# Kernel tuning notes

Measured on AMD Instinct MI355X. Metric: run time of the kernel, lower is better.

Reference implementation:

```python
import jax, jax.numpy as jnp
import numpy as np

B, T, D_IN, P, Q, D_OUT = 128, 1024, 64, 128, 2, 64


def _lstm_layer(x, w_ih, w_hh, b):
    """One LSTM layer, batch_first. x: [B,T,Din], w_ih: [4P,Din], w_hh: [4P,P], b: [4P].
    PyTorch gate order: i, f, g, o."""
    # Precompute input contribution for all timesteps (the big, parallel GEMM).
    gx = jnp.einsum('btd,gd->btg', x, w_ih) + b          # [B,T,4P]
    gx_t = jnp.swapaxes(gx, 0, 1)                        # [T,B,4P] for scan
    p = w_hh.shape[1]
    h0 = jnp.zeros((x.shape[0], p), dtype=x.dtype)
    c0 = jnp.zeros((x.shape[0], p), dtype=x.dtype)

    def step(carry, g_in):
        h, c = carry
        g = g_in + h @ w_hh.T                            # [B,4P]
        i, f, gg, o = jnp.split(g, 4, axis=-1)
        i = jax.nn.sigmoid(i)
        f = jax.nn.sigmoid(f)
        gg = jnp.tanh(gg)
        o = jax.nn.sigmoid(o)
        c = f * c + i * gg
        h = o * jnp.tanh(c)
        return (h, c), h

    _, hs = jax.lax.scan(step, (h0, c0), gx_t)           # hs: [T,B,P]
    return jnp.swapaxes(hs, 0, 1)                        # [B,T,P]


def setup_inputs() -> dict:
    key = jax.random.key(0)
    ks = jax.random.split(key, 8)
    x = jax.random.normal(ks[0], (B, T, D_IN), dtype=jnp.float32)
    # weight_ih: kaiming-normal-ish; weight_hh: orthogonal-ish (random normal is a fine stand-in
    # numerically; init distribution doesn't change the math being tested).
    w_ih0 = jax.random.normal(ks[1], (4 * P, D_IN), dtype=jnp.float32) * (1.0 / np.sqrt(D_IN))
    w_hh0 = jax.random.normal(ks[2], (4 * P, P), dtype=jnp.float32) * (1.0 / np.sqrt(P))
    w_ih1 = jax.random.normal(ks[3], (4 * P, P), dtype=jnp.float32) * (1.0 / np.sqrt(P))
    w_hh1 = jax.random.normal(ks[4], (4 * P, P), dtype=jnp.float32) * (1.0 / np.sqrt(P))
    # biases initialized to zero in the original (bias_ih + bias_hh folded into one per layer
    # would be equivalent math; keep both for faithfulness)
    b_ih = jnp.zeros((Q, 4 * P), dtype=jnp.float32)
    b_hh = jnp.zeros((Q, 4 * P), dtype=jnp.float32)
    fc_w = jax.random.normal(ks[5], (D_OUT, P), dtype=jnp.float32) * np.sqrt(2.0 / P)
    fc_b = jnp.zeros((D_OUT,), dtype=jnp.float32)
    return {"x": x, "w_ih0": w_ih0, "w_hh0": w_hh0, "w_ih1": w_ih1, "w_hh1": w_hh1,
            "b_ih": b_ih, "b_hh": b_hh, "fc_w": fc_w, "fc_b": fc_b}


def reference(x, w_ih0, w_hh0, w_ih1, w_hh1, b_ih, b_hh, fc_w, fc_b):
    h = _lstm_layer(x, w_ih0, w_hh0, b_ih[0] + b_hh[0])   # layer 0: [B,T,P]
    h = _lstm_layer(h, w_ih1, w_hh1, b_ih[1] + b_hh[1])   # layer 1: [B,T,P]
    return jnp.einsum('btp,op->bto', h, fc_w) + fc_b      # [B,T,D_OUT]
```

## Files before the change

kernel.cpp:

```cpp
#include <hip/hip_runtime.h>

#define NT 1024
#define RINGS 256

typedef _Float16 half8 __attribute__((ext_vector_type(8)));
typedef _Float16 half4 __attribute__((ext_vector_type(4)));
typedef float f32x4 __attribute__((ext_vector_type(4)));
typedef unsigned long long u64;
struct U2 { u64 a, b; };

#ifndef __has_builtin
#define __has_builtin(x) 0
#endif

__device__ __forceinline__ f32x4 MFMA(half8 a, half8 b, f32x4 c) {
  return __builtin_amdgcn_mfma_f32_16x16x32_f16(a, b, c, 0, 0, 0);
}
__device__ __forceinline__ float exp2h(float x) {
#if __has_builtin(__builtin_amdgcn_exp2f)
  return __builtin_amdgcn_exp2f(x);
#else
  return exp2f(x);
#endif
}
__device__ __forceinline__ float sigf(float x) {
  return __builtin_amdgcn_rcpf(1.0f + exp2h(x * -1.44269504f));
}
__device__ __forceinline__ float tanhf2(float x) {
  float t = __builtin_amdgcn_rcpf(1.0f + exp2h(x * 2.88539008f));
  return fmaf(-2.0f, t, 1.0f);
}
__device__ __forceinline__ half8 cvt8(float4 c0, float4 c1) {
  half8 hv;
  hv[0] = (_Float16)c0.x; hv[1] = (_Float16)c0.y;
  hv[2] = (_Float16)c0.z; hv[3] = (_Float16)c0.w;
  hv[4] = (_Float16)c1.x; hv[5] = (_Float16)c1.y;
  hv[6] = (_Float16)c1.z; hv[7] = (_Float16)c1.w;
  return hv;
}
__device__ __forceinline__ half8 ldring(const _Float16* p) {
  const u64* q = (const u64*)p;
  U2 uu;
  uu.a = __hip_atomic_load(q, __ATOMIC_RELAXED, __HIP_MEMORY_SCOPE_AGENT);
  uu.b = __hip_atomic_load(q + 1, __ATOMIC_RELAXED, __HIP_MEMORY_SCOPE_AGENT);
  return __builtin_bit_cast(half8, uu);
}
__device__ __forceinline__ unsigned wpoll(unsigned* p, unsigned tgt,
                                          unsigned cached, int l) {
  unsigned c = cached;
  while (c < tgt) {
    unsigned pv = 0;
    if (l == 0)
      pv = __hip_atomic_load(p, __ATOMIC_ACQUIRE, __HIP_MEMORY_SCOPE_AGENT);
    c = (unsigned)__builtin_amdgcn_readfirstlane((int)pv);
    if (c < tgt) __builtin_amdgcn_s_sleep(2);
  }
  return c;
}

__global__ __launch_bounds__(256) void prep_x(const float* __restrict__ x,
                                              _Float16* __restrict__ Xf) {
  int t0 = blockIdx.x * 256 + threadIdx.x;
  int l = t0 & 63;
  int fid = t0 >> 6;
  int kt = fid & 1;
  int t = (fid >> 1) & (NT - 1);
  int g = fid >> 11;
  int bt = g * 16 + (l & 15);
  int kb = kt * 32 + (l >> 4) * 4;
  const float* src = x + ((size_t)bt * NT + (size_t)t) * 64 + kb;
  float4 v0 = *(const float4*)src;
  float4 v1 = *(const float4*)(src + 16);
  *(half8*)(Xf + (size_t)fid * 512 + l * 8) = cvt8(v0, v1);
}

__global__ __launch_bounds__(512, 1) void lstm_main(
    const float* __restrict__ wih0, const float* __restrict__ whh0,
    const float* __restrict__ wih1, const float* __restrict__ whh1,
    const float* __restrict__ bih, const float* __restrict__ bhh,
    const float* __restrict__ fcw, const float* __restrict__ fcb,
    const _Float16* __restrict__ Xf, _Float16* __restrict__ ringH0,
    unsigned* __restrict__ flags, float* __restrict__ out) {
  const int tid = threadIdx.x;
  const int w = tid >> 6, l = tid & 63;
  const int n = l & 15, lg = l >> 4;
  const bool producer = blockIdx.x < 8;
  const int g = blockIdx.x & 7;

  __shared__ _Float16 hfr[2][4][64][8];
  __shared__ _Float16 fcl[4][4][64][8];

  _Float16* ringG = ringH0 + (size_t)g * RINGS * 2048;
  unsigned* prog = flags + g * 16;
  unsigned* cons = flags + (8 + g) * 16;
  const half8 hz = {0, 0, 0, 0, 0, 0, 0, 0};

  if (producer) {
    half8 A[4][6];
    f32x4 bias[4];
#pragma unroll
    for (int q = 0; q < 4; ++q) {
      int row = (w + 8 * q) * 16 + n;
#pragma unroll
      for (int kt = 0; kt < 2; ++kt) {
        const float* wp = wih0 + (size_t)row * 64 + kt * 32 + lg * 4;
        A[q][kt] = cvt8(*(const float4*)wp, *(const float4*)(wp + 16));
      }
#pragma unroll
      for (int kt = 0; kt < 4; ++kt) {
        const float* wp = whh0 + (size_t)row * 128 + kt * 32 + lg * 4;
        A[q][2 + kt] = cvt8(*(const float4*)wp, *(const float4*)(wp + 16));
      }
      int rb = (w + 8 * q) * 16 + lg * 4;
      f32x4 bv;
#pragma unroll
      for (int r = 0; r < 4; ++r) bv[r] = bih[rb + r] + bhh[rb + r];
      bias[q] = bv;
    }
    if (tid < 256) ((half8*)&hfr[1][0][0][0])[tid] = hz;
    const _Float16* XfG = Xf + (size_t)g * NT * 1024;
    f32x4 cst = {0.f, 0.f, 0.f, 0.f};
    unsigned Cc = 0;
    half8 x0 = *(const half8*)(XfG + l * 8);
    half8 x1 = *(const half8*)(XfG + 512 + l * 8);
    f32x4 xs0 = MFMA(A[0][0], x0, bias[0]);
    f32x4 xs1 = MFMA(A[1][0], x0, bias[1]);
    f32x4 xs2 = MFMA(A[2][0], x0, bias[2]);
    f32x4 xs3 = MFMA(A[3][0], x0, bias[3]);
    xs0 = MFMA(A[0][1], x1, xs0); xs1 = MFMA(A[1][1], x1, xs1);
    xs2 = MFMA(A[2][1], x1, xs2); xs3 = MFMA(A[3][1], x1, xs3);
    half8 xC0 = *(const half8*)(XfG + 1024 + l * 8);
    half8 xC1 = *(const half8*)(XfG + 1024 + 512 + l * 8);
    __syncthreads();
    for (int s = 0; s < NT; ++s) {
      if (s >= 224 && (s & 31) == 0)
        Cc = wpoll(cons, (unsigned)(s - 192), Cc, l);
      const int rdk = (s + 1) & 1;
      half8 b2 = *(const half8*)&hfr[rdk][0][l][0];
      half8 b3 = *(const half8*)&hfr[rdk][1][l][0];
      half8 b4 = *(const half8*)&hfr[rdk][2][l][0];
      half8 b5 = *(const half8*)&hfr[rdk][3][l][0];
      f32x4 hc0 = MFMA(A[0][2], b2, xs0);
      f32x4 hc1 = MFMA(A[1][2], b2, xs1);
      f32x4 hc2 = MFMA(A[2][2], b2, xs2);
      f32x4 hc3 = MFMA(A[3][2], b2, xs3);
      hc0 = MFMA(A[0][3], b3, hc0); hc1 = MFMA(A[1][3], b3, hc1);
      hc2 = MFMA(A[2][3], b3, hc2); hc3 = MFMA(A[3][3], b3, hc3);
      hc0 = MFMA(A[0][4], b4, hc0); hc1 = MFMA(A[1][4], b4, hc1);
      hc2 = MFMA(A[2][4], b4, hc2); hc3 = MFMA(A[3][4], b4, hc3);
      hc0 = MFMA(A[0][5], b5, hc0); hc1 = MFMA(A[1][5], b5, hc1);
      hc2 = MFMA(A[2][5], b5, hc2); hc3 = MFMA(A[3][5], b5, hc3);
      if (s + 1 < NT) {
        xs0 = MFMA(A[0][0], xC0, bias[0]);
        xs1 = MFMA(A[1][0], xC0, bias[1]);
        xs2 = MFMA(A[2][0], xC0, bias[2]);
        xs3 = MFMA(A[3][0], xC0, bias[3]);
        xs0 = MFMA(A[0][1], xC1, xs0); xs1 = MFMA(A[1][1], xC1, xs1);
        xs2 = MFMA(A[2][1], xC1, xs2); xs3 = MFMA(A[3][1], xC1, xs3);
      }
      if (s + 2 < NT) {
        const _Float16* p = XfG + (size_t)(s + 2) * 1024 + l * 8;
        xC0 = *(const half8*)p;
        xC1 = *(const half8*)(p + 512);
      }
      half4 hh;
#pragma unroll
      for (int r = 0; r < 4; ++r) {
        float iv = sigf(hc0[r]), fv = sigf(hc1[r]);
        float gv = tanhf2(hc2[r]), ov = sigf(hc3[r]);
        cst[r] = fv * cst[r] + iv * gv;
        hh[r] = (_Float16)(ov * tanhf2(cst[r]));
      }
      *(half4*)&hfr[s & 1][w >> 1][l][(w & 1) << 2] = hh;
      {
        u64 uh = __builtin_bit_cast(u64, hh);
        __hip_atomic_store(
            (u64*)(ringG + (size_t)(s & (RINGS - 1)) * 2048 +
                   (w >> 1) * 512 + l * 8 + (w & 1) * 4),
            uh, __ATOMIC_RELAXED, __HIP_MEMORY_SCOPE_AGENT);
      }
      asm volatile("s_waitcnt lgkmcnt(0)" ::: "memory");
      __builtin_amdgcn_sched_barrier(0);
      __builtin_amdgcn_s_barrier();
      __builtin_amdgcn_sched_barrier(0);
      if ((s & 31) == 31) {
        asm volatile("s_waitcnt vmcnt(0)" ::: "memory");
        __builtin_amdgcn_sched_barrier(0);
        __builtin_amdgcn_s_barrier();
        __builtin_amdgcn_sched_barrier(0);
        if (tid == 0)
          __hip_atomic_store(prog, (unsigned)(s + 1), __ATOMIC_RELEASE,
                             __HIP_MEMORY_SCOPE_AGENT);
      }
    }
  } else {
    half8 A[4][8];
    f32x4 bias[4], fcbv = {0.f, 0.f, 0.f, 0.f};
#pragma unroll
    for (int q = 0; q < 4; ++q) {
      int row = (w + 8 * q) * 16 + n;
#pragma unroll
      for (int kt = 0; kt < 4; ++kt) {
        const float* wp = wih1 + (size_t)row * 128 + kt * 32 + lg * 4;
        A[q][kt] = cvt8(*(const float4*)wp, *(const float4*)(wp + 16));
      }
#pragma unroll
      for (int kt = 0; kt < 4; ++kt) {
        const float* wp = whh1 + (size_t)row * 128 + kt * 32 + lg * 4;
        A[q][4 + kt] = cvt8(*(const float4*)wp, *(const float4*)(wp + 16));
      }
      int rb = (w + 8 * q) * 16 + lg * 4;
      f32x4 bv;
#pragma unroll
      for (int r = 0; r < 4; ++r)
        bv[r] = bih[512 + rb + r] + bhh[512 + rb + r];
      bias[q] = bv;
    }
    if (w < 4) {
      int frow = (w << 4) + n;
#pragma unroll
      for (int kt = 0; kt < 4; ++kt) {
        const float* wp = fcw + (size_t)frow * 128 + kt * 32 + lg * 4;
        *(half8*)&fcl[w][kt][l][0] =
            cvt8(*(const float4*)wp, *(const float4*)(wp + 16));
      }
      fcbv = *(const f32x4*)(fcb + (w << 4) + lg * 4);
    }
    if (tid < 256) ((half8*)&hfr[1][0][0][0])[tid] = hz;
    float* outG = out + (size_t)((g << 4) + n) * NT * 64 + (w << 4) + lg * 4;
    f32x4 cst = {0.f, 0.f, 0.f, 0.f};
    __syncthreads();
    unsigned Pc = wpoll(prog, 2u, 0u, l);
    half8 t0 = ldring(ringG + l * 8);
    half8 t1 = ldring(ringG + 512 + l * 8);
    half8 t2 = ldring(ringG + 1024 + l * 8);
    half8 t3 = ldring(ringG + 1536 + l * 8);
    f32x4 is0 = MFMA(A[0][0], t0, bias[0]);
    f32x4 is1 = MFMA(A[1][0], t0, bias[1]);
    f32x4 is2 = MFMA(A[2][0], t0, bias[2]);
    f32x4 is3 = MFMA(A[3][0], t0, bias[3]);
    is0 = MFMA(A[0][1], t1, is0); is1 = MFMA(A[1][1], t1, is1);
    is2 = MFMA(A[2][1], t1, is2); is3 = MFMA(A[3][1], t1, is3);
    is0 = MFMA(A[0][2], t2, is0); is1 = MFMA(A[1][2], t2, is1);
    is2 = MFMA(A[2][2], t2, is2); is3 = MFMA(A[3][2], t2, is3);
    is0 = MFMA(A[0][3], t3, is0); is1 = MFMA(A[1][3], t3, is1);
    is2 = MFMA(A[2][3], t3, is2); is3 = MFMA(A[3][3], t3, is3);
    const _Float16* rb1 = ringG + 2048 + l * 8;
    half8 HC0 = ldring(rb1);
    half8 HC1 = ldring(rb1 + 512);
    half8 HC2 = ldring(rb1 + 1024);
    half8 HC3 = ldring(rb1 + 1536);
    for (int t = 0; t < NT; ++t) {
      const int rdk = (t + 1) & 1;
      half8 b4 = *(const half8*)&hfr[rdk][0][l][0];
      half8 b5 = *(const half8*)&hfr[rdk][1][l][0];
      half8 b6 = *(const half8*)&hfr[rdk][2][l][0];
      half8 b7 = *(const half8*)&hfr[rdk][3][l][0];
      f32x4 hc0 = MFMA(A[0][4], b4, is0);
      f32x4 hc1 = MFMA(A[1][4], b4, is1);
      f32x4 hc2 = MFMA(A[2][4], b4, is2);
      f32x4 hc3 = MFMA(A[3][4], b4, is3);
      hc0 = MFMA(A[0][5], b5, hc0); hc1 = MFMA(A[1][5], b5, hc1);
      hc2 = MFMA(A[2][5], b5, hc2); hc3 = MFMA(A[3][5], b5, hc3);
      hc0 = MFMA(A[0][6], b6, hc0); hc1 = MFMA(A[1][6], b6, hc1);
      hc2 = MFMA(A[2][6], b6, hc2); hc3 = MFMA(A[3][6], b6, hc3);
      hc0 = MFMA(A[0][7], b7, hc0); hc1 = MFMA(A[1][7], b7, hc1);
      hc2 = MFMA(A[2][7], b7, hc2); hc3 = MFMA(A[3][7], b7, hc3);
      if (w < 4) {
        half8 f0 = *(const half8*)&fcl[w][0][l][0];
        half8 f1 = *(const half8*)&fcl[w][1][l][0];
        half8 f2 = *(const half8*)&fcl[w][2][l][0];
        half8 f3 = *(const half8*)&fcl[w][3][l][0];
        f32x4 afc = fcbv;
        afc = MFMA(f0, b4, afc); afc = MFMA(f1, b5, afc);
        afc = MFMA(f2, b6, afc); afc = MFMA(f3, b7, afc);
        if (t >= 1) *(f32x4*)(outG + (size_t)(t - 1) * 64) = afc;
      }
      if (t + 1 < NT) {
        is0 = MFMA(A[0][0], HC0, bias[0]);
        is1 = MFMA(A[1][0], HC0, bias[1]);
        is2 = MFMA(A[2][0], HC0, bias[2]);
        is3 = MFMA(A[3][0], HC0, bias[3]);
        is0 = MFMA(A[0][1], HC1, is0); is1 = MFMA(A[1][1], HC1, is1);
        is2 = MFMA(A[2][1], HC1, is2); is3 = MFMA(A[3][1], HC1, is3);
        is0 = MFMA(A[0][2], HC2, is0); is1 = MFMA(A[1][2], HC2, is1);
        is2 = MFMA(A[2][2], HC2, is2); is3 = MFMA(A[3][2], HC2, is3);
        is0 = MFMA(A[0][3], HC3, is0); is1 = MFMA(A[1][3], HC3, is1);
        is2 = MFMA(A[2][3], HC3, is2); is3 = MFMA(A[3][3], HC3, is3);
      }
      if (t + 2 < NT) {
        Pc = wpoll(prog, (unsigned)(t + 3), Pc, l);
        const _Float16* rb_ =
            ringG + (size_t)((t + 2) & (RINGS - 1)) * 2048 + l * 8;
        HC0 = ldring(rb_);
        HC1 = ldring(rb_ + 512);
        HC2 = ldring(rb_ + 1024);
        HC3 = ldring(rb_ + 1536);
      }
      half4 hh;
#pragma unroll
      for (int r = 0; r < 4; ++r) {
        float iv = sigf(hc0[r]), fv = sigf(hc1[r]);
        float gv = tanhf2(hc2[r]), ov = sigf(hc3[r]);
        cst[r] = fv * cst[r] + iv * gv;
        hh[r] = (_Float16)(ov * tanhf2(cst[r]));
      }
      *(half4*)&hfr[t & 1][w >> 1][l][(w & 1) << 2] = hh;
      if (tid == 0 && (t & 31) == 0)
        __hip_atomic_store(cons, (unsigned)t, __ATOMIC_RELAXED,
                           __HIP_MEMORY_SCOPE_AGENT);
      asm volatile("s_waitcnt lgkmcnt(0)" ::: "memory");
      __builtin_amdgcn_sched_barrier(0);
      __builtin_amdgcn_s_barrier();
      __builtin_amdgcn_sched_barrier(0);
    }
    {
      half8 b4 = *(const half8*)&hfr[(NT + 1) & 1][0][l][0];
      half8 b5 = *(const half8*)&hfr[(NT + 1) & 1][1][l][0];
      half8 b6 = *(const half8*)&hfr[(NT + 1) & 1][2][l][0];
      half8 b7 = *(const half8*)&hfr[(NT + 1) & 1][3][l][0];
      if (w < 4) {
        half8 f0 = *(const half8*)&fcl[w][0][l][0];
        half8 f1 = *(const half8*)&fcl[w][1][l][0];
        half8 f2 = *(const half8*)&fcl[w][2][l][0];
        half8 f3 = *(const half8*)&fcl[w][3][l][0];
        f32x4 afc = fcbv;
        afc = MFMA(f0, b4, afc); afc = MFMA(f1, b5, afc);
        afc = MFMA(f2, b6, afc); afc = MFMA(f3, b7, afc);
        *(f32x4*)(outG + (size_t)(NT - 1) * 64) = afc;
      }
    }
  }
}

extern "C" void kernel_launch(void* const* d_in, const int* in_sizes, int n_in,
                              void* d_out, int out_size, void* d_ws, size_t ws_size,
                              hipStream_t stream) {
  const float* x     = (const float*)d_in[0];
  const float* w_ih0 = (const float*)d_in[1];
  const float* w_hh0 = (const float*)d_in[2];
  const float* w_ih1 = (const float*)d_in[3];
  const float* w_hh1 = (const float*)d_in[4];
  const float* b_ih  = (const float*)d_in[5];
  const float* b_hh  = (const float*)d_in[6];
  const float* fc_w  = (const float*)d_in[7];
  const float* fc_b  = (const float*)d_in[8];

  _Float16* Xf   = (_Float16*)d_ws;
  _Float16* ring = (_Float16*)((char*)d_ws + (16u << 20));
  unsigned* flags = (unsigned*)((char*)d_ws + (24u << 20));

  hipMemsetAsync(flags, 0, 4096, stream);
  prep_x<<<4096, 256, 0, stream>>>(x, Xf);
  lstm_main<<<16, 512, 0, stream>>>(w_ih0, w_hh0, w_ih1, w_hh1, b_ih, b_hh,
                                    fc_w, fc_b, Xf, ring, flags,
                                    (float*)d_out);
}
```

Baseline: 1.328 ms.

## Split each block into input-projection and recurrent warp groups via LDS handoff

Result: slower. 1.616 ms (+21.7%).

```diff
diff --git a/kernel.cpp b/kernel.cpp
--- a/kernel.cpp
+++ b/kernel.cpp
@@ -74,7 +74,13 @@
   *(half8*)(Xf + (size_t)fid * 512 + l * 8) = cvt8(v0, v1);
 }
 
-__global__ __launch_bounds__(512, 1) void lstm_main(
+#define BARRIER_LGKM()                              \
+  asm volatile("s_waitcnt lgkmcnt(0)" ::: "memory"); \
+  __builtin_amdgcn_sched_barrier(0);                 \
+  __builtin_amdgcn_s_barrier();                      \
+  __builtin_amdgcn_sched_barrier(0)
+
+__global__ __launch_bounds__(1024, 1) void lstm_main(
     const float* __restrict__ wih0, const float* __restrict__ whh0,
     const float* __restrict__ wih1, const float* __restrict__ whh1,
     const float* __restrict__ bih, const float* __restrict__ bhh,
@@ -86,248 +92,294 @@
   const int n = l & 15, lg = l >> 4;
   const bool producer = blockIdx.x < 8;
   const int g = blockIdx.x & 7;
+  const int q = w & 7;
 
   __shared__ _Float16 hfr[2][4][64][8];
-  __shared__ _Float16 fcl[4][4][64][8];
+  __shared__ float pp[2][8][4][64][4];
 
   _Float16* ringG = ringH0 + (size_t)g * RINGS * 2048;
   unsigned* prog = flags + g * 16;
   unsigned* cons = flags + (8 + g) * 16;
   const half8 hz = {0, 0, 0, 0, 0, 0, 0, 0};
 
+  if (tid < 256) ((half8*)&hfr[1][0][0][0])[tid] = hz;
+
   if (producer) {
-    half8 A[4][6];
-    f32x4 bias[4];
-#pragma unroll
-    for (int q = 0; q < 4; ++q) {
-      int row = (w + 8 * q) * 16 + n;
-#pragma unroll
-      for (int kt = 0; kt < 2; ++kt) {
-        const float* wp = wih0 + (size_t)row * 64 + kt * 32 + lg * 4;
-        A[q][kt] = cvt8(*(const float4*)wp, *(const float4*)(wp + 16));
-      }
-#pragma unroll
-      for (int kt = 0; kt < 4; ++kt) {
-        const float* wp = whh0 + (size_t)row * 128 + kt * 32 + lg * 4;
-        A[q][2 + kt] = cvt8(*(const float4*)wp, *(const float4*)(wp + 16));
-      }
-      int rb = (w + 8 * q) * 16 + lg * 4;
-      f32x4 bv;
-#pragma unroll
-      for (int r = 0; r < 4; ++r) bv[r] = bih[rb + r] + bhh[rb + r];
-      bias[q] = bv;
-    }
-    if (tid < 256) ((half8*)&hfr[1][0][0][0])[tid] = hz;
-    const _Float16* XfG = Xf + (size_t)g * NT * 1024;
-    f32x4 cst = {0.f, 0.f, 0.f, 0.f};
-    unsigned Cc = 0;
-    half8 x0 = *(const half8*)(XfG + l * 8);
-    half8 x1 = *(const half8*)(XfG + 512 + l * 8);
-    f32x4 xs0 = MFMA(A[0][0], x0, bias[0]);
-    f32x4 xs1 = MFMA(A[1][0], x0, bias[1]);
-    f32x4 xs2 = MFMA(A[2][0], x0, bias[2]);
-    f32x4 xs3 = MFMA(A[3][0], x0, bias[3]);
-    xs0 = MFMA(A[0][1], x1, xs0); xs1 = MFMA(A[1][1], x1, xs1);
-    xs2 = MFMA(A[2][1], x1, xs2); xs3 = MFMA(A[3][1], x1, xs3);
-    half8 xC0 = *(const half8*)(XfG + 1024 + l * 8);
-    half8 xC1 = *(const half8*)(XfG + 1024 + 512 + l * 8);
-    __syncthreads();
-    for (int s = 0; s < NT; ++s) {
-      if (s >= 224 && (s & 31) == 0)
-        Cc = wpoll(cons, (unsigned)(s - 192), Cc, l);
-      const int rdk = (s + 1) & 1;
-      half8 b2 = *(const half8*)&hfr[rdk][0][l][0];
-      half8 b3 = *(const half8*)&hfr[rdk][1][l][0];
-      half8 b4 = *(const half8*)&hfr[rdk][2][l][0];
-      half8 b5 = *(const half8*)&hfr[rdk][3][l][0];
-      f32x4 hc0 = MFMA(A[0][2], b2, xs0);
-      f32x4 hc1 = MFMA(A[1][2], b2, xs1);
-      f32x4 hc2 = MFMA(A[2][2], b2, xs2);
-      f32x4 hc3 = MFMA(A[3][2], b2, xs3);
-      hc0 = MFMA(A[0][3], b3, hc0); hc1 = MFMA(A[1][3], b3, hc1);
-      hc2 = MFMA(A[2][3], b3, hc2); hc3 = MFMA(A[3][3], b3, hc3);
-      hc0 = MFMA(A[0][4], b4, hc0); hc1 = MFMA(A[1][4], b4, hc1);
-      hc2 = MFMA(A[2][4], b4, hc2); hc3 = MFMA(A[3][4], b4, hc3);
-      hc0 = MFMA(A[0][5], b5, hc0); hc1 = MFMA(A[1][5], b5, hc1);
-      hc2 = MFMA(A[2][5], b5, hc2); hc3 = MFMA(A[3][5], b5, hc3);
-      if (s + 1 < NT) {
-        xs0 = MFMA(A[0][0], xC0, bias[0]);
-        xs1 = MFMA(A[1][0], xC0, bias[1]);
-        xs2 = MFMA(A[2][0], xC0, bias[2]);
-        xs3 = MFMA(A[3][0], xC0, bias[3]);
-        xs0 = MFMA(A[0][1], xC1, xs0); xs1 = MFMA(A[1][1], xC1, xs1);
-        xs2 = MFMA(A[2][1], xC1, xs2); xs3 = MFMA(A[3][1], xC1, xs3);
-      }
-      if (s + 2 < NT) {
-        const _Float16* p = XfG + (size_t)(s + 2) * 1024 + l * 8;
-        xC0 = *(const half8*)p;
-        xC1 = *(const half8*)(p + 512);
-      }
-      half4 hh;
-#pragma unroll
-      for (int r = 0; r < 4; ++r) {
-        float iv = sigf(hc0[r]), fv = sigf(hc1[r]);
-        float gv = tanhf2(hc2[r]), ov = sigf(hc3[r]);
-        cst[r] = fv * cst[r] + iv * gv;
-        hh[r] = (_Float16)(ov * tanhf2(cst[r]));
-      }
-      *(half4*)&hfr[s & 1][w >> 1][l][(w & 1) << 2] = hh;
+    if (w < 8) {
+      half8 Ax[4][2];
+      f32x4 bias[4];
+#pragma unroll
+      for (int gt = 0; gt < 4; ++gt) {
+        int row = (q + 8 * gt) * 16 + n;
+#pragma unroll
+        for (int kt = 0; kt < 2; ++kt) {
+          const float* wp = wih0 + (size_t)row * 64 + kt * 32 + lg * 4;
+          Ax[gt][kt] = cvt8(*(const float4*)wp, *(const float4*)(wp + 16));
+        }
+        int rb = (q + 8 * gt) * 16 + lg * 4;
+        f32x4 bv;
+#pragma unroll
+        for (int r = 0; r < 4; ++r) bv[r] = bih[rb + r] + bhh[rb + r];
+        bias[gt] = bv;
+      }
+      const _Float16* XfG = Xf + (size_t)g * NT * 1024;
+      half8 xv0 = *(const half8*)(XfG + l * 8);
+      half8 xv1 = *(const half8*)(XfG + 512 + l * 8);
       {
+        f32x4 a0 = MFMA(Ax[0][0], xv0, bias[0]);
+        f32x4 a1 = MFMA(Ax[1][0], xv0, bias[1]);
+        f32x4 a2 = MFMA(Ax[2][0], xv0, bias[2]);
+        f32x4 a3 = MFMA(Ax[3][0], xv0, bias[3]);
+        a0 = MFMA(Ax[0][1], xv1, a0); a1 = MFMA(Ax[1][1], xv1, a1);
+        a2 = MFMA(Ax[2][1], xv1, a2); a3 = MFMA(Ax[3][1], xv1, a3);
+        *(f32x4*)&pp[0][q][0][l][0] = a0;
+        *(f32x4*)&pp[0][q][1][l][0] = a1;
+        *(f32x4*)&pp[0][q][2][l][0] = a2;
+        *(f32x4*)&pp[0][q][3][l][0] = a3;
+      }
+      xv0 = *(const half8*)(XfG + 1024 + l * 8);
+      xv1 = *(const half8*)(XfG + 1024 + 512 + l * 8);
+      unsigned Cc = 0;
+      __syncthreads();
+      for (int s = 0; s < NT; ++s) {
+        if (s >= 224 && (s & 31) == 0)
+          Cc = wpoll(cons, (unsigned)(s - 192), Cc, l);
+        if (s + 1 < NT) {
+          f32x4 a0 = MFMA(Ax[0][0], xv0, bias[0]);
+          f32x4 a1 = MFMA(Ax[1][0], xv0, bias[1]);
+          f32x4 a2 = MFMA(Ax[2][0], xv0, bias[2]);
+          f32x4 a3 = MFMA(Ax[3][0], xv0, bias[3]);
+          a0 = MFMA(Ax[0][1], xv1, a0); a1 = MFMA(Ax[1][1], xv1, a1);
+          a2 = MFMA(Ax[2][1], xv1, a2); a3 = MFMA(Ax[3][1], xv1, a3);
+          const int sl = (s + 1) & 1;
+          *(f32x4*)&pp[sl][q][0][l][0] = a0;
+          *(f32x4*)&pp[sl][q][1][l][0] = a1;
+          *(f32x4*)&pp[sl][q][2][l][0] = a2;
+          *(f32x4*)&pp[sl][q][3][l][0] = a3;
+        }
+        if (s + 2 < NT) {
+          const _Float16* p = XfG + (size_t)(s + 2) * 1024 + l * 8;
+          xv0 = *(const half8*)p;
+          xv1 = *(const half8*)(p + 512);
+        }
+        BARRIER_LGKM();
+        if ((s & 31) == 31) {
+          asm volatile("s_waitcnt vmcnt(0)" ::: "memory");
+          __builtin_amdgcn_sched_barrier(0);
+          __builtin_amdgcn_s_barrier();
+          __builtin_amdgcn_sched_barrier(0);
+          if (tid == 0)
+            __hip_atomic_store(prog, (unsigned)(s + 1), __ATOMIC_RELEASE,
+                               __HIP_MEMORY_SCOPE_AGENT);
+        }
+      }
+    } else {
+      half8 Ah[4][4];
+#pragma unroll
+      for (int gt = 0; gt < 4; ++gt) {
+        int row = (q + 8 * gt) * 16 + n;
+#pragma unroll
+        for (int kt = 0; kt < 4; ++kt) {
+          const float* wp = whh0 + (size_t)row * 128 + kt * 32 + lg * 4;
+          Ah[gt][kt] = cvt8(*(const float4*)wp, *(const float4*)(wp + 16));
+        }
+      }
+      f32x4 cst = {0.f, 0.f, 0.f, 0.f};
+      unsigned Cc = 0;
+      __syncthreads();
+      for (int s = 0; s < NT; ++s) {
+        if (s >= 224 && (s & 31) == 0)
+          Cc = wpoll(cons, (unsigned)(s - 192), Cc, l);
+        const int rdk = (s + 1) & 1;
+        half8 b0 = *(const half8*)&hfr[rdk][0][l][0];
+        half8 b1 = *(const half8*)&hfr[rdk][1][l][0];
+        half8 b2 = *(const half8*)&hfr[rdk][2][l][0];
+        half8 b3 = *(const half8*)&hfr[rdk][3][l][0];
+        f32x4 c0 = *(const f32x4*)&pp[s & 1][q][0][l][0];
+        f32x4 c1 = *(const f32x4*)&pp[s & 1][q][1][l][0];
+        f32x4 c2 = *(const f32x4*)&pp[s & 1][q][2][l][0];
+        f32x4 c3 = *(const f32x4*)&pp[s & 1][q][3][l][0];
+        c0 = MFMA(Ah[0][0], b0, c0); c1 = MFMA(Ah[1][0], b0, c1);
+        c2 = MFMA(Ah[2][0], b0, c2); c3 = MFMA(Ah[3][0], b0, c3);
+        c0 = MFMA(Ah[0][1], b1, c0); c1 = MFMA(Ah[1][1], b1, c1);
+        c2 = MFMA(Ah[2][1], b1, c2); c3 = MFMA(Ah[3][1], b1, c3);
+        c0 = MFMA(Ah[0][2], b2, c0); c1 = MFMA(Ah[1][2], b2, c1);
+        c2 = MFMA(Ah[2][2], b2, c2); c3 = MFMA(Ah[3][2], b2, c3);
+        c0 = MFMA(Ah[0][3], b3, c0); c1 = MFMA(Ah[1][3], b3, c1);
+        c2 = MFMA(Ah[2][3], b3, c2); c3 = MFMA(Ah[3][3], b3, c3);
+        half4 hh;
+#pragma unroll
+        for (int r = 0; r < 4; ++r) {
+          float iv = sigf(c0[r]), fv = sigf(c1[r]);
+          float gv = tanhf2(c2[r]), ov = sigf(c3[r]);
+          cst[r] = fv * cst[r] + iv * gv;
+          hh[r] = (_Float16)(ov * tanhf2(cst[r]));
+        }
+        *(half4*)&hfr[s & 1][q >> 1][l][(q & 1) << 2] = hh;
         u64 uh = __builtin_bit_cast(u64, hh);
         __hip_atomic_store(
             (u64*)(ringG + (size_t)(s & (RINGS - 1)) * 2048 +
-                   (w >> 1) * 512 + l * 8 + (w & 1) * 4),
+                   (q >> 1) * 512 + l * 8 + (q & 1) * 4),
             uh, __ATOMIC_RELAXED, __HIP_MEMORY_SCOPE_AGENT);
-      }
-      asm volatile("s_waitcnt lgkmcnt(0)" ::: "memory");
-      __builtin_amdgcn_sched_barrier(0);
-      __builtin_amdgcn_s_barrier();
-      __builtin_amdgcn_sched_barrier(0);
-      if ((s & 31) == 31) {
-        asm volatile("s_waitcnt vmcnt(0)" ::: "memory");
-        __builtin_amdgcn_sched_barrier(0);
-        __builtin_amdgcn_s_barrier();
-        __builtin_amdgcn_sched_barrier(0);
-        if (tid == 0)
-          __hip_atomic_store(prog, (unsigned)(s + 1), __ATOMIC_RELEASE,
-                             __HIP_MEMORY_SCOPE_AGENT);
+        BARRIER_LGKM();
+        if ((s & 31) == 31) {
+          asm volatile("s_waitcnt vmcnt(0)" ::: "memory");
+          __builtin_amdgcn_sched_barrier(0);
+          __builtin_amdgcn_s_barrier();
+          __builtin_amdgcn_sched_barrier(0);
+        }
       }
     }
   } else {
-    half8 A[4][8];
-    f32x4 bias[4], fcbv = {0.f, 0.f, 0.f, 0.f};
-#pragma unroll
-    for (int q = 0; q < 4; ++q) {
-      int row = (w + 8 * q) * 16 + n;
-#pragma unroll
-      for (int kt = 0; kt < 4; ++kt) {
-        const float* wp = wih1 + (size_t)row * 128 + kt * 32 + lg * 4;
-        A[q][kt] = cvt8(*(const float4*)wp, *(const float4*)(wp + 16));
-      }
-#pragma unroll
-      for (int kt = 0; kt < 4; ++kt) {
-        const float* wp = whh1 + (size_t)row * 128 + kt * 32 + lg * 4;
-        A[q][4 + kt] = cvt8(*(const float4*)wp, *(const float4*)(wp + 16));
-      }
-      int rb = (w + 8 * q) * 16 + lg * 4;
-      f32x4 bv;
-#pragma unroll
-      for (int r = 0; r < 4; ++r)
-        bv[r] = bih[512 + rb + r] + bhh[512 + rb + r];
-      bias[q] = bv;
-    }
-    if (w < 4) {
-      int frow = (w << 4) + n;
-#pragma unroll
-      for (int kt = 0; kt < 4; ++kt) {
-        const float* wp = fcw + (size_t)frow * 128 + kt * 32 + lg * 4;
-        *(half8*)&fcl[w][kt][l][0] =
-            cvt8(*(const float4*)wp, *(const float4*)(wp + 16));
-      }
-      fcbv = *(const f32x4*)(fcb + (w << 4) + lg * 4);
-    }
-    if (tid < 256) ((half8*)&hfr[1][0][0][0])[tid] = hz;
-    float* outG = out + (size_t)((g << 4) + n) * NT * 64 + (w << 4) + lg * 4;
-    f32x4 cst = {0.f, 0.f, 0.f, 0.f};
-    __syncthreads();
-    unsigned Pc = wpoll(prog, 2u, 0u, l);
-    half8 t0 = ldring(ringG + l * 8);
-    half8 t1 = ldring(ringG + 512 + l * 8);
-    half8 t2 = ldring(ringG + 1024 + l * 8);
-    half8 t3 = ldring(ringG + 1536 + l * 8);
-    f32x4 is0 = MFMA(A[0][0], t0, bias[0]);
-    f32x4 is1 = MFMA(A[1][0], t0, bias[1]);
-    f32x4 is2 = MFMA(A[2][0], t0, bias[2]);
-    f32x4 is3 = MFMA(A[3][0], t0, bias[3]);
-    is0 = MFMA(A[0][1], t1, is0); is1 = MFMA(A[1][1], t1, is1);
-    is2 = MFMA(A[2][1], t1, is2); is3 = MFMA(A[3][1], t1, is3);
-    is0 = MFMA(A[0][2], t2, is0); is1 = MFMA(A[1][2], t2, is1);
-    is2 = MFMA(A[2][2], t2, is2); is3 = MFMA(A[3][2], t2, is3);
-    is0 = MFMA(A[0][3], t3, is0); is1 = MFMA(A[1][3], t3, is1);
-    is2 = MFMA(A[2][3], t3, is2); is3 = MFMA(A[3][3], t3, is3);
-    const _Float16* rb1 = ringG + 2048 + l * 8;
-    half8 HC0 = ldring(rb1);
-    half8 HC1 = ldring(rb1 + 512);
-    half8 HC2 = ldring(rb1 + 1024);
-    half8 HC3 = ldring(rb1 + 1536);
-    for (int t = 0; t < NT; ++t) {
-      const int rdk = (t + 1) & 1;
-      half8 b4 = *(const half8*)&hfr[rdk][0][l][0];
-      half8 b5 = *(const half8*)&hfr[rdk][1][l][0];
-      half8 b6 = *(const half8*)&hfr[rdk][2][l][0];
-      half8 b7 = *(const half8*)&hfr[rdk][3][l][0];
-      f32x4 hc0 = MFMA(A[0][4], b4, is0);
-      f32x4 hc1 = MFMA(A[1][4], b4, is1);
-      f32x4 hc2 = MFMA(A[2][4], b4, is2);
-      f32x4 hc3 = MFMA(A[3][4], b4, is3);
-      hc0 = MFMA(A[0][5], b5, hc0); hc1 = MFMA(A[1][5], b5, hc1);
-      hc2 = MFMA(A[2][5], b5, hc2); hc3 = MFMA(A[3][5], b5, hc3);
-      hc0 = MFMA(A[0][6], b6, hc0); hc1 = MFMA(A[1][6], b6, hc1);
-      hc2 = MFMA(A[2][6], b6, hc2); hc3 = MFMA(A[3][6], b6, hc3);
-      hc0 = MFMA(A[0][7], b7, hc0); hc1 = MFMA(A[1][7], b7, hc1);
-      hc2 = MFMA(A[2][7], b7, hc2); hc3 = MFMA(A[3][7], b7, hc3);
-      if (w < 4) {
-        half8 f0 = *(const half8*)&fcl[w][0][l][0];
-        half8 f1 = *(const half8*)&fcl[w][1][l][0];
-        half8 f2 = *(const half8*)&fcl[w][2][l][0];
-        half8 f3 = *(const half8*)&fcl[w][3][l][0];
-        f32x4 afc = fcbv;
-        afc = MFMA(f0, b4, afc); afc = MFMA(f1, b5, afc);
-        afc = MFMA(f2, b6, afc); afc = MFMA(f3, b7, afc);
-        if (t >= 1) *(f32x4*)(outG + (size_t)(t - 1) * 64) = afc;
-      }
-      if (t + 1 < NT) {
-        is0 = MFMA(A[0][0], HC0, bias[0]);
-        is1 = MFMA(A[1][0], HC0, bias[1]);
-        is2 = MFMA(A[2][0], HC0, bias[2]);
-        is3 = MFMA(A[3][0], HC0, bias[3]);
-        is0 = MFMA(A[0][1], HC1, is0); is1 = MFMA(A[1][1], HC1, is1);
-        is2 = MFMA(A[2][1], HC1, is2); is3 = MFMA(A[3][1], HC1, is3);
-        is0 = MFMA(A[0][2], HC2, is0); is1 = MFMA(A[1][2], HC2, is1);
-        is2 = MFMA(A[2][2], HC2, is2); is3 = MFMA(A[3][2], HC2, is3);
-        is0 = MFMA(A[0][3], HC3, is0); is1 = MFMA(A[1][3], HC3, is1);
-        is2 = MFMA(A[2][3], HC3, is2); is3 = MFMA(A[3][3], HC3, is3);
-      }
-      if (t + 2 < NT) {
-        Pc = wpoll(prog, (unsigned)(t + 3), Pc, l);
-        const _Float16* rb_ =
-            ringG + (size_t)((t + 2) & (RINGS - 1)) * 2048 + l * 8;
-        HC0 = ldring(rb_);
-        HC1 = ldring(rb_ + 512);
-        HC2 = ldring(rb_ + 1024);
-        HC3 = ldring(rb_ + 1536);
-      }
-      half4 hh;
-#pragma unroll
-      for (int r = 0; r < 4; ++r) {
-        float iv = sigf(hc0[r]), fv = sigf(hc1[r]);
-        float gv = tanhf2(hc2[r]), ov = sigf(hc3[r]);
-        cst[r] = fv * cst[r] + iv * gv;
-        hh[r] = (_Float16)(ov * tanhf2(cst[r]));
-      }
-      *(half4*)&hfr[t & 1][w >> 1][l][(w & 1) << 2] = hh;
-      if (tid == 0 && (t & 31) == 0)
-        __hip_atomic_store(cons, (unsigned)t, __ATOMIC_RELAXED,
-                           __HIP_MEMORY_SCOPE_AGENT);
-      asm volatile("s_waitcnt lgkmcnt(0)" ::: "memory");
-      __builtin_amdgcn_sched_barrier(0);
-      __builtin_amdgcn_s_barrier();
-      __builtin_amdgcn_sched_barrier(0);
-    }
-    {
-      half8 b4 = *(const half8*)&hfr[(NT + 1) & 1][0][l][0];
-      half8 b5 = *(const half8*)&hfr[(NT + 1) & 1][1][l][0];
-      half8 b6 = *(const half8*)&hfr[(NT + 1) & 1][2][l][0];
-      half8 b7 = *(const half8*)&hfr[(NT + 1) & 1][3][l][0];
-      if (w < 4) {
-        half8 f0 = *(const half8*)&fcl[w][0][l][0];
-        half8 f1 = *(const half8*)&fcl[w][1][l][0];
-        half8 f2 = *(const half8*)&fcl[w][2][l][0];
-        half8 f3 = *(const half8*)&fcl[w][3][l][0];
-        f32x4 afc = fcbv;
-        afc = MFMA(f0, b4, afc); afc = MFMA(f1, b5, afc);
-        afc = MFMA(f2, b6, afc); afc = MFMA(f3, b7, afc);
-        *(f32x4*)(outG + (size_t)(NT - 1) * 64) = afc;
+    if (w < 8) {
+      half8 Ai[4][4];
+      f32x4 bias[4];
+#pragma unroll
+      for (int gt = 0; gt < 4; ++gt) {
+        int row = (q + 8 * gt) * 16 + n;
+#pragma unroll
+        for (int kt = 0; kt < 4; ++kt) {
+          const float* wp = wih1 + (size_t)row * 128 + kt * 32 + lg * 4;
+          Ai[gt][kt] = cvt8(*(const float4*)wp, *(const float4*)(wp + 16));
+        }
+        int rb = (q + 8 * gt) * 16 + lg * 4;
+        f32x4 bv;
+#pragma unroll
+        for (int r = 0; r < 4; ++r)
+          bv[r] = bih[512 + rb + r] + bhh[512 + rb + r];
+        bias[gt] = bv;
+      }
+      unsigned Pc = wpoll(prog, 2u, 0u, l);
+      half8 t0 = ldring(ringG + l * 8);
+      half8 t1 = ldring(ringG + 512 + l * 8);
+      half8 t2 = ldring(ringG + 1024 + l * 8);
+      half8 t3 = ldring(ringG + 1536 + l * 8);
+      {
+        f32x4 a0 = MFMA(Ai[0][0], t0, bias[0]);
+        f32x4 a1 = MFMA(Ai[1][0], t0, bias[1]);
+        f32x4 a2 = MFMA(Ai[2][0], t0, bias[2]);
+        f32x4 a3 = MFMA(Ai[3][0], t0, bias[3]);
+        a0 = MFMA(Ai[0][1], t1, a0); a1 = MFMA(Ai[1][1], t1, a1);
+        a2 = MFMA(Ai[2][1], t1, a2); a3 = MFMA(Ai[3][1], t1, a3);
+        a0 = MFMA(Ai[0][2], t2, a0); a1 = MFMA(Ai[1][2], t2, a1);
+        a2 = MFMA(Ai[2][2], t2, a2); a3 = MFMA(Ai[3][2], t2, a3);
+        a0 = MFMA(Ai[0][3], t3, a0); a1 = MFMA(Ai[1][3], t3, a1);
+        a2 = MFMA(Ai[2][3], t3, a2); a3 = MFMA(Ai[3][3], t3, a3);
+        *(f32x4*)&pp[0][q][0][l][0] = a0;
+        *(f32x4*)&pp[0][q][1][l][0] = a1;
+        *(f32x4*)&pp[0][q][2][l][0] = a2;
+        *(f32x4*)&pp[0][q][3][l][0] = a3;
+      }
+      const _Float16* rb1 = ringG + 2048 + l * 8;
+      half8 HC0 = ldring(rb1);
+      half8 HC1 = ldring(rb1 + 512);
+      half8 HC2 = ldring(rb1 + 1024);
+      half8 HC3 = ldring(rb1 + 1536);
+      __syncthreads();
+      for (int t = 0; t < NT; ++t) {
+        if (t + 1 < NT) {
+          f32x4 a0 = MFMA(Ai[0][0], HC0, bias[0]);
+          f32x4 a1 = MFMA(Ai[1][0], HC0, bias[1]);
+          f32x4 a2 = MFMA(Ai[2][0], HC0, bias[2]);
+          f32x4 a3 = MFMA(Ai[3][0], HC0, bias[3]);
+          a0 = MFMA(Ai[0][1], HC1, a0); a1 = MFMA(Ai[1][1], HC1, a1);
+          a2 = MFMA(Ai[2][1], HC1, a2); a3 = MFMA(Ai[3][1], HC1, a3);
+          a0 = MFMA(Ai[0][2], HC2, a0); a1 = MFMA(Ai[1][2], HC2, a1);
+          a2 = MFMA(Ai[2][2], HC2, a2); a3 = MFMA(Ai[3][2], HC2, a3);
+          a0 = MFMA(Ai[0][3], HC3, a0); a1 = MFMA(Ai[1][3], HC3, a1);
+          a2 = MFMA(Ai[2][3], HC3, a2); a3 = MFMA(Ai[3][3], HC3, a3);
+          const int sl = (t + 1) & 1;
+          *(f32x4*)&pp[sl][q][0][l][0] = a0;
+          *(f32x4*)&pp[sl][q][1][l][0] = a1;
+          *(f32x4*)&pp[sl][q][2][l][0] = a2;
+          *(f32x4*)&pp[sl][q][3][l][0] = a3;
+        }
+        if (t + 2 < NT) {
+          Pc = wpoll(prog, (unsigned)(t + 3), Pc, l);
+          const _Float16* rb_ =
+              ringG + (size_t)((t + 2) & (RINGS - 1)) * 2048 + l * 8;
+          HC0 = ldring(rb_);
+          HC1 = ldring(rb_ + 512);
+          HC2 = ldring(rb_ + 1024);
+          HC3 = ldring(rb_ + 1536);
+        }
+        BARRIER_LGKM();
+      }
+    } else {
+      half8 Ah[4][4], FCA[4];
+      f32x4 fcbv = {0.f, 0.f, 0.f, 0.f};
+#pragma unroll
+      for (int gt = 0; gt < 4; ++gt) {
+        int row = (q + 8 * gt) * 16 + n;
+#pragma unroll
+        for (int kt = 0; kt < 4; ++kt) {
+          const float* wp = whh1 + (size_t)row * 128 + kt * 32 + lg * 4;
+          Ah[gt][kt] = cvt8(*(const float4*)wp, *(const float4*)(wp + 16));
+        }
+      }
+      const bool fcw_ = (q < 4);
+      if (fcw_) {
+        int frow = (q << 4) + n;
+#pragma unroll
+        for (int kt = 0; kt < 4; ++kt) {
+          const float* wp = fcw + (size_t)frow * 128 + kt * 32 + lg * 4;
+          FCA[kt] = cvt8(*(const float4*)wp, *(const float4*)(wp + 16));
+        }
+        fcbv = *(const f32x4*)(fcb + (q << 4) + lg * 4);
+      }
+      float* outG = out + (size_t)((g << 4) + n) * NT * 64 + (q << 4) + lg * 4;
+      f32x4 cst = {0.f, 0.f, 0.f, 0.f};
+      __syncthreads();
+      for (int t = 0; t < NT; ++t) {
+        const int rdk = (t + 1) & 1;
+        half8 b0 = *(const half8*)&hfr[rdk][0][l][0];
+        half8 b1 = *(const half8*)&hfr[rdk][1][l][0];
+        half8 b2 = *(const half8*)&hfr[rdk][2][l][0];
+        half8 b3 = *(const half8*)&hfr[rdk][3][l][0];
+        f32x4 c0 = *(const f32x4*)&pp[t & 1][q][0][l][0];
+        f32x4 c1 = *(const f32x4*)&pp[t & 1][q][1][l][0];
+        f32x4 c2 = *(const f32x4*)&pp[t & 1][q][2][l][0];
+        f32x4 c3 = *(const f32x4*)&pp[t & 1][q][3][l][0];
+        c0 = MFMA(Ah[0][0], b0, c0); c1 = MFMA(Ah[1][0], b0, c1);
+        c2 = MFMA(Ah[2][0], b0, c2); c3 = MFMA(Ah[3][0], b0, c3);
+        c0 = MFMA(Ah[0][1], b1, c0); c1 = MFMA(Ah[1][1], b1, c1);
+        c2 = MFMA(Ah[2][1], b1, c2); c3 = MFMA(Ah[3][1], b1, c3);
+        c0 = MFMA(Ah[0][2], b2, c0); c1 = MFMA(Ah[1][2], b2, c1);
+        c2 = MFMA(Ah[2][2], b2, c2); c3 = MFMA(Ah[3][2], b2, c3);
+        c0 = MFMA(Ah[0][3], b3, c0); c1 = MFMA(Ah[1][3], b3, c1);
+        c2 = MFMA(Ah[2][3], b3, c2); c3 = MFMA(Ah[3][3], b3, c3);
+        if (fcw_) {
+          f32x4 afc = fcbv;
+          afc = MFMA(FCA[0], b0, afc); afc = MFMA(FCA[1], b1, afc);
+          afc = MFMA(FCA[2], b2, afc); afc = MFMA(FCA[3], b3, afc);
+          if (t >= 1) *(f32x4*)(outG + (size_t)(t - 1) * 64) = afc;
+        }
+        half4 hh;
+#pragma unroll
+        for (int r = 0; r < 4; ++r) {
+          float iv = sigf(c0[r]), fv = sigf(c1[r]);
+          float gv = tanhf2(c2[r]), ov = sigf(c3[r]);
+          cst[r] = fv * cst[r] + iv * gv;
+          hh[r] = (_Float16)(ov * tanhf2(cst[r]));
+        }
+        *(half4*)&hfr[t & 1][q >> 1][l][(q & 1) << 2] = hh;
+        if (tid == 512 && (t & 31) == 0)
+          __hip_atomic_store(cons, (unsigned)t, __ATOMIC_RELAXED,
+                             __HIP_MEMORY_SCOPE_AGENT);
+        BARRIER_LGKM();
+      }
+      {
+        const int rdk = (NT + 1) & 1;
+        half8 b0 = *(const half8*)&hfr[rdk][0][l][0];
+        half8 b1 = *(const half8*)&hfr[rdk][1][l][0];
+        half8 b2 = *(const half8*)&hfr[rdk][2][l][0];
+        half8 b3 = *(const half8*)&hfr[rdk][3][l][0];
+        if (fcw_) {
+          f32x4 afc = fcbv;
+          afc = MFMA(FCA[0], b0, afc); afc = MFMA(FCA[1], b1, afc);
+          afc = MFMA(FCA[2], b2, afc); afc = MFMA(FCA[3], b3, afc);
+          *(f32x4*)(outG + (size_t)(NT - 1) * 64) = afc;
+        }
       }
     }
   }
@@ -350,9 +402,9 @@
   _Float16* ring = (_Float16*)((char*)d_ws + (16u << 20));
   unsigned* flags = (unsigned*)((char*)d_ws + (24u << 20));
 
-  hipMemsetAsync(flags, 0, 4096, stream);
+  (void)hipMemsetAsync(flags, 0, 4096, stream);
   prep_x<<<4096, 256, 0, stream>>>(x, Xf);
-  lstm_main<<<16, 512, 0, stream>>>(w_ih0, w_hh0, w_ih1, w_hh1, b_ih, b_hh,
-                                    fc_w, fc_b, Xf, ring, flags,
-                                    (float*)d_out);
-}
+  lstm_main<<<16, 1024, 0, stream>>>(w_ih0, w_hh0, w_ih1, w_hh1, b_ih, b_hh,
+                                     fc_w, fc_b, Xf, ring, flags,
+                                     (float*)d_out);
+}
```
